# Optimization experiments

Measured on AMD Instinct MI355X. Metric: run time of the kernel, lower is better.

## Reference

```python
import jax, jax.numpy as jnp
import numpy as np

NUM_EXPERTS = 64
TOP_K = 2
TEMPERATURE = 1.0
MOMENTUM = 0.9


def _l2norm(x, axis=-1):
    # torch F.normalize: x / max(||x||, eps)
    n = jnp.linalg.norm(x, axis=axis, keepdims=True)
    return x / jnp.maximum(n, 1e-12)


def setup_inputs() -> dict:
    key = jax.random.key(0)
    k1, k2 = jax.random.split(key)
    hidden_states = jax.random.normal(k1, (4, 4096, 2048), dtype=jnp.float32)
    centers = _l2norm(jax.random.normal(k2, (NUM_EXPERTS, 2048), dtype=jnp.float32))
    return {"hidden_states": hidden_states, "centers": centers}


def reference(hidden_states, centers):
    B, T, H = hidden_states.shape
    flat = hidden_states.reshape(-1, H).astype(jnp.float32)  # [N, H]
    N = flat.shape[0]

    # cosine-similarity logits
    reps_n = _l2norm(flat)
    centers_n = _l2norm(centers)
    temp = jnp.maximum(jnp.float32(TEMPERATURE), 1e-6)
    logits = (reps_n @ centers_n.T) / temp  # [N, E]

    probs = jax.nn.softmax(logits, axis=-1)
    top_w, top_ids = jax.lax.top_k(probs, TOP_K)  # [N, k]
    top_w = top_w / (jnp.sum(top_w, axis=-1, keepdims=True) + 1e-9)

    # EMA center update from top-1 routed expert (training+update path)
    route = top_ids[:, 0]  # [N]
    sums = jax.ops.segment_sum(flat, route, num_segments=NUM_EXPERTS)  # [E, H]
    counts = jax.ops.segment_sum(jnp.ones((N, 1), jnp.float32), route,
                                 num_segments=NUM_EXPERTS)  # [E, 1]
    means = sums / (counts + 1e-6)
    updated = _l2norm(MOMENTUM * centers + (1.0 - MOMENTUM) * means)
    new_centers = jnp.where(counts > 0, updated, centers)

    top_ids = top_ids.reshape(B, T, TOP_K)
    top_w = top_w.reshape(B, T, TOP_K)
    return top_ids, top_w, new_centers
```

## Files before the change

### kernel.cpp

```cpp
#include <hip/hip_runtime.h>
#include <math.h>

#define NTOK 16384
#define HDIM 2048
#define NEXP 64
#define KK   32
#define TAU  5e-5f
#define LGT  16384
#define MAXB 2048
#define KPAD 40
#define LTS  132

typedef __attribute__((ext_vector_type(8))) short short8;
typedef __attribute__((ext_vector_type(4))) float f32x4;
typedef __attribute__((ext_vector_type(2))) unsigned int uint2v;


__global__ __launch_bounds__(256)
void zero_kernel(float* p, int n) {
  int i = blockIdx.x * 256 + threadIdx.x;
  if (i < n) p[i] = 0.0f;
}

__device__ __forceinline__ float block_reduce_sum(float v, float* red) {
  #pragma unroll
  for (int o = 32; o > 0; o >>= 1) v += __shfl_down(v, o, 64);
  int lane = threadIdx.x & 63;
  int wid  = threadIdx.x >> 6;
  if (lane == 0) red[wid] = v;
  __syncthreads();
  float s = red[0] + red[1] + red[2] + red[3];
  __syncthreads();
  return s;
}

__device__ __forceinline__ double block_reduce_sum_f64(double v, double* red) {
  const int tid = threadIdx.x;
  red[tid] = v;
  __syncthreads();
  if (tid < 128) red[tid] += red[tid + 128];
  __syncthreads();
  if (tid < 64)  red[tid] += red[tid + 64];
  __syncthreads();
  double s = 0.0;
  if (tid < 64) {
    s = red[tid];
    #pragma unroll
    for (int o = 32; o > 0; o >>= 1) s += __shfl_down(s, o, 64);
  }
  if (tid == 0) red[0] = s;
  __syncthreads();
  s = red[0];
  __syncthreads();
  return s;
}

__global__ __launch_bounds__(256)
void cnorm_kernel(const float* __restrict__ c, float* __restrict__ inv_nc) {
  __shared__ float red[4];
  int e = blockIdx.x;
  float ss = 0.f;
  #pragma unroll
  for (int j = 0; j < 8; ++j) {
    float v = c[e * HDIM + threadIdx.x + j * 256];
    ss += v * v;
  }
  float tot = block_reduce_sum(ss, red);
  if (threadIdx.x == 0) inv_nc[e] = 1.0f / fmaxf(sqrtf(tot), 1e-12f);
}

__global__ __launch_bounds__(256)
void cnormalize_kernel(const float* __restrict__ c, float* __restrict__ bn) {
  __shared__ double redd[256];
  __shared__ float s_nc;
  const int e = blockIdx.x;
  const int tid = threadIdx.x;
  const float* cr = c + (size_t)e * HDIM;
  double acc = 0.0;
  #pragma unroll
  for (int i = 0; i < 8; ++i) {
    double v = (double)cr[tid + 256 * i];
    acc += v * v;
  }
  double cn = block_reduce_sum_f64(acc, redd);
  if (tid == 0) s_nc = (float)fmax(sqrt(cn), 1e-12);
  __syncthreads();
  const double nc = (double)s_nc;
  #pragma unroll
  for (int i = 0; i < 8; ++i) {
    int k = tid + 256 * i;
    bn[(size_t)e * HDIM + k] = (float)((double)cr[k] / nc);
  }
}

__device__ __forceinline__ void cvt2(float v0, float v1, unsigned &hi, unsigned &lo) {
  unsigned u0 = __float_as_uint(v0);
  unsigned u1 = __float_as_uint(v1);
  unsigned h0 = u0 & 0xffff0000u;
  unsigned h1 = u1 & 0xffff0000u;
  float r0 = v0 - __uint_as_float(h0);
  float r1 = v1 - __uint_as_float(h1);
  hi = (u0 >> 16) | h1;
  lo = (__float_as_uint(r0) >> 16) | (__float_as_uint(r1) & 0xffff0000u);
}

__global__ __launch_bounds__(256)
void gemm_kernel(const float* __restrict__ x, const float* __restrict__ c,
                 float* __restrict__ logits, float* __restrict__ xnorm2) {
  __shared__ __align__(16) unsigned short smem[15360];
  unsigned short (*Ah)[KPAD] = (unsigned short (*)[KPAD])(smem);
  unsigned short (*Al)[KPAD] = (unsigned short (*)[KPAD])(smem + 5120);
  unsigned short (*Bh)[KPAD] = (unsigned short (*)[KPAD])(smem + 10240);
  unsigned short (*Bl)[KPAD] = (unsigned short (*)[KPAD])(smem + 12800);

  const int tid  = threadIdx.x;
  const int mt   = blockIdx.x >> 2;
  const int ks   = blockIdx.x & 3;
  const int t0   = mt * 128;
  const int kb   = ks * 512;
  const int sr   = tid >> 1;
  const int sq   = (tid & 1) * 16;
  const int er   = tid >> 2;
  const int eq   = (tid & 3) * 8;
  const int lane = tid & 63;
  const int w    = tid >> 6;
  const int fr   = lane & 15;
  const int fk   = (lane >> 4) * 8;

  const float* xrow = x + (size_t)(t0 + sr) * HDIM + kb + sq;
  const float* crow = c + (size_t)er * HDIM + kb + eq;

  f32x4 xp[4], cp[2];
  #pragma unroll
  for (int i = 0; i < 4; ++i) xp[i] = *(const f32x4*)(xrow + 4 * i);
  #pragma unroll
  for (int i = 0; i < 2; ++i) cp[i] = *(const f32x4*)(crow + 4 * i);

  f32x4 acc[2][4];
  #pragma unroll
  for (int mi = 0; mi < 2; ++mi)
    #pragma unroll
    for (int ni = 0; ni < 4; ++ni)
      acc[mi][ni] = (f32x4){0.f, 0.f, 0.f, 0.f};
  float nacc = 0.f;

  for (int it = 0; it < 16; ++it) {
    __syncthreads();
    #pragma unroll
    for (int i = 0; i < 4; ++i) {
      unsigned h01, l01, h23, l23;
      cvt2(xp[i].x, xp[i].y, h01, l01);
      cvt2(xp[i].z, xp[i].w, h23, l23);
      *(uint2v*)&Ah[sr][sq + 4 * i] = (uint2v){h01, h23};
      *(uint2v*)&Al[sr][sq + 4 * i] = (uint2v){l01, l23};
      nacc += xp[i].x*xp[i].x + xp[i].y*xp[i].y + xp[i].z*xp[i].z + xp[i].w*xp[i].w;
    }
    #pragma unroll
    for (int i = 0; i < 2; ++i) {
      unsigned h01, l01, h23, l23;
      cvt2(cp[i].x, cp[i].y, h01, l01);
      cvt2(cp[i].z, cp[i].w, h23, l23);
      *(uint2v*)&Bh[er][eq + 4 * i] = (uint2v){h01, h23};
      *(uint2v*)&Bl[er][eq + 4 * i] = (uint2v){l01, l23};
    }
    __syncthreads();
    if (it < 15) {
      const float* xn = xrow + (it + 1) * KK;
      const float* cn = crow + (it + 1) * KK;
      #pragma unroll
      for (int i = 0; i < 4; ++i) xp[i] = *(const f32x4*)(xn + 4 * i);
      #pragma unroll
      for (int i = 0; i < 2; ++i) cp[i] = *(const f32x4*)(cn + 4 * i);
    }
    short8 ah0 = *(const short8*)&Ah[w * 32 + fr][fk];
    short8 ah1 = *(const short8*)&Ah[w * 32 + 16 + fr][fk];
    short8 al0 = *(const short8*)&Al[w * 32 + fr][fk];
    short8 al1 = *(const short8*)&Al[w * 32 + 16 + fr][fk];
    #pragma unroll
    for (int ni = 0; ni < 4; ++ni) {
      short8 bh = *(const short8*)&Bh[ni * 16 + fr][fk];
      short8 bl = *(const short8*)&Bl[ni * 16 + fr][fk];
      acc[0][ni] = __builtin_amdgcn_mfma_f32_16x16x32_bf16(ah0, bh, acc[0][ni], 0, 0, 0);
      acc[0][ni] = __builtin_amdgcn_mfma_f32_16x16x32_bf16(ah0, bl, acc[0][ni], 0, 0, 0);
      acc[0][ni] = __builtin_amdgcn_mfma_f32_16x16x32_bf16(al0, bh, acc[0][ni], 0, 0, 0);
      acc[1][ni] = __builtin_amdgcn_mfma_f32_16x16x32_bf16(ah1, bh, acc[1][ni], 0, 0, 0);
      acc[1][ni] = __builtin_amdgcn_mfma_f32_16x16x32_bf16(ah1, bl, acc[1][ni], 0, 0, 0);
      acc[1][ni] = __builtin_amdgcn_mfma_f32_16x16x32_bf16(al1, bh, acc[1][ni], 0, 0, 0);
    }
  }

  atomicAdd(&xnorm2[t0 + sr], nacc);

  float* lt = (float*)smem;
  #pragma unroll
  for (int eh = 0; eh < 2; ++eh) {
    __syncthreads();
    #pragma unroll
    for (int ni2 = 0; ni2 < 2; ++ni2) {
      const int ni = eh * 2 + ni2;
      const int e  = ni2 * 16 + fr;
      #pragma unroll
      for (int mi = 0; mi < 2; ++mi) {
        const int t = w * 32 + mi * 16 + (lane >> 4) * 4;
        *(f32x4*)&lt[e * LTS + t] = acc[mi][ni];
      }
    }
    __syncthreads();
    #pragma unroll
    for (int n = 0; n < 16; ++n) {
      const int f = tid + n * 256;
      const int e = f >> 7;
      const int t = f & 127;
      atomicAdd(&logits[(size_t)(e + eh * 32) * LGT + t0 + t], lt[e * LTS + t]);
    }
  }
}

__global__ __launch_bounds__(64)
void softmax_kernel(const float* __restrict__ logits, const float* __restrict__ xnorm2,
                    const float* __restrict__ inv_nc, float* __restrict__ out,
                    int* __restrict__ route, int* __restrict__ nflag,
                    int* __restrict__ flags) {
  __shared__ float snc[NEXP];
  const int tid = threadIdx.x;
  snc[tid] = inv_nc[tid];
  __syncthreads();
  const int t = blockIdx.x * 64 + tid;
  const float inv_nx = 1.0f / fmaxf(sqrtf(xnorm2[t]), 1e-12f);
  float lv[NEXP];
  #pragma unroll
  for (int e = 0; e < NEXP; ++e)
    lv[e] = logits[(size_t)e * LGT + t] * snc[e] * inv_nx;
  float m1 = -1e30f, m2 = -1e30f, m3 = -1e30f;
  int i1 = 0, i2 = 0;
  #pragma unroll
  for (int e = 0; e < NEXP; ++e) {
    float l = lv[e];
    if (l > m1)      { m3 = m2; m2 = m1; i2 = i1; m1 = l; i1 = e; }
    else if (l > m2) { m3 = m2; m2 = l; i2 = e; }
    else if (l > m3) { m3 = l; }
  }
  float Z = 0.f;
  #pragma unroll
  for (int e = 0; e < NEXP; ++e) Z += expf(lv[e] - m1);
  const float p1w = 1.0f / Z;
  const float p2w = expf(m2 - m1) / Z;
  const float s   = p1w + p2w + 1e-9f;
  out[t * 2 + 0] = (float)i1;
  out[t * 2 + 1] = (float)i2;
  out[2 * NTOK + t * 2 + 0] = p1w / s;
  out[2 * NTOK + t * 2 + 1] = p2w / s;
  route[t] = i1;
  if ((m1 - m2) < TAU || (m2 - m3) < TAU) {
    int idx = atomicAdd(nflag, 1);
    flags[idx] = t;
  }
}

__global__ __launch_bounds__(256)
void refine_np_kernel(const float* __restrict__ x, const float* __restrict__ bn,
                      float* __restrict__ out, int* __restrict__ route,
                      const int* __restrict__ nflag, const int* __restrict__ flags) {
  __shared__ float a_lds[HDIM];
  __shared__ double redd[256];
  __shared__ float lf[NEXP];
  __shared__ float s_nx;
  const int tid  = threadIdx.x;
  const int lane = tid & 63;
  const int w    = tid >> 6;
  const int n = *nflag;
  for (int j = blockIdx.x; j < n; j += gridDim.x) {
    const int t = flags[j];
    const float* xr = x + (size_t)t * HDIM;
    double xacc = 0.0;
    #pragma unroll
    for (int i = 0; i < 8; ++i) {
      double v = (double)xr[tid + 256 * i];
      xacc += v * v;
    }
    double xn = block_reduce_sum_f64(xacc, redd);
    if (tid == 0) s_nx = (float)fmax(sqrt(xn), 1e-12);
    __syncthreads();
    const double nx = (double)s_nx;
    #pragma unroll
    for (int i = 0; i < 8; ++i) {
      int k = tid + 256 * i;
      a_lds[k] = (float)((double)xr[k] / nx);
    }
    __syncthreads();
    #pragma unroll 1
    for (int ei = 0; ei < 16; ++ei) {
      const int e = w * 16 + ei;
      const float* br = bn + (size_t)e * HDIM;
      double d = 0.0;
      #pragma unroll 8
      for (int i = 0; i < 32; ++i) {
        int k = lane + 64 * i;
        d += (double)a_lds[k] * (double)br[k];
      }
      #pragma unroll
      for (int o = 32; o > 0; o >>= 1) d += __shfl_down(d, o, 64);
      if (lane == 0) lf[e] = (float)d;
    }
    __syncthreads();
    if (tid == 0) {
      float m32 = lf[0];
      for (int ee = 1; ee < NEXP; ++ee) m32 = fmaxf(m32, lf[ee]);
      float ex[NEXP];
      for (int ee = 0; ee < NEXP; ++ee)
        ex[ee] = (float)exp((double)(lf[ee] - m32));
      float r[8];
      #pragma unroll
      for (int q = 0; q < 8; ++q) r[q] = ex[q];
      for (int i = 8; i < NEXP; i += 8)
        #pragma unroll
        for (int q = 0; q < 8; ++q) r[q] += ex[i + q];
      const float Z = ((r[0] + r[1]) + (r[2] + r[3])) + ((r[4] + r[5]) + (r[6] + r[7]));
      float p1 = -1.f, p2 = -1.f;
      int i1 = 0, i2 = 0;
      for (int ee = 0; ee < NEXP; ++ee) {
        float p = ex[ee] / Z;
        if (p > p1)      { p2 = p1; i2 = i1; p1 = p; i1 = ee; }
        else if (p > p2) { p2 = p; i2 = ee; }
      }
      const float s = (p1 + p2) + 1e-9f;
      out[t * 2 + 0] = (float)i1;
      out[t * 2 + 1] = (float)i2;
      out[2 * NTOK + t * 2 + 0] = p1 / s;
      out[2 * NTOK + t * 2 + 1] = p2 / s;
      route[t] = i1;
    }
    __syncthreads();
  }
}

__global__ __launch_bounds__(64)
void refine_np_slow(const float* __restrict__ x, const float* __restrict__ c,
                    float* __restrict__ out, int* __restrict__ route,
                    const int* __restrict__ nflag, const int* __restrict__ flags) {
  __shared__ float lf[NEXP];
  const int e = threadIdx.x;
  const int n = *nflag;
  for (int j = blockIdx.x; j < n; j += gridDim.x) {
    const int t = flags[j];
    const float* xr = x + (size_t)t * HDIM;
    const float* cr = c + (size_t)e * HDIM;
    double xn = 0.0, cn = 0.0;
    for (int k = 0; k < HDIM; ++k) {
      double xv = (double)xr[k];
      double cv = (double)cr[k];
      xn += xv * xv;
      cn += cv * cv;
    }
    const float nx32 = (float)fmax(sqrt(xn), 1e-12);
    const float nc32 = (float)fmax(sqrt(cn), 1e-12);
    double d = 0.0;
    for (int k = 0; k < HDIM; ++k) {
      float a = (float)((double)xr[k] / (double)nx32);
      float b = (float)((double)cr[k] / (double)nc32);
      d += (double)a * (double)b;
    }
    lf[e] = (float)d;
    __syncthreads();
    if (e == 0) {
      float m32 = lf[0];
      for (int ee = 1; ee < NEXP; ++ee) m32 = fmaxf(m32, lf[ee]);
      float ex[NEXP];
      for (int ee = 0; ee < NEXP; ++ee)
        ex[ee] = (float)exp((double)(lf[ee] - m32));
      float r[8];
      #pragma unroll
      for (int q = 0; q < 8; ++q) r[q] = ex[q];
      for (int i = 8; i < NEXP; i += 8)
        #pragma unroll
        for (int q = 0; q < 8; ++q) r[q] += ex[i + q];
      const float Z = ((r[0] + r[1]) + (r[2] + r[3])) + ((r[4] + r[5]) + (r[6] + r[7]));
      float p1 = -1.f, p2 = -1.f;
      int i1 = 0, i2 = 0;
      for (int ee = 0; ee < NEXP; ++ee) {
        float p = ex[ee] / Z;
        if (p > p1)      { p2 = p1; i2 = i1; p1 = p; i1 = ee; }
        else if (p > p2) { p2 = p; i2 = ee; }
      }
      const float s = (p1 + p2) + 1e-9f;
      out[t * 2 + 0] = (float)i1;
      out[t * 2 + 1] = (float)i2;
      out[2 * NTOK + t * 2 + 0] = p1 / s;
      out[2 * NTOK + t * 2 + 1] = p2 / s;
      route[t] = i1;
    }
    __syncthreads();
  }
}

__global__ __launch_bounds__(256)
void scatter_kernel(const int* __restrict__ route, int* __restrict__ cursor,
                    int* __restrict__ bucket) {
  const int t = blockIdx.x * 256 + threadIdx.x;
  const int e = route[t];
  const int pos = atomicAdd(&cursor[e], 1);
  if (pos < MAXB) bucket[e * MAXB + pos] = t;
}

__global__ __launch_bounds__(256)
void segsum_dense(const float* __restrict__ x, const int* __restrict__ cursor,
                  const int* __restrict__ bucket, float* __restrict__ sums) {
  __shared__ int ts[MAXB];
  const int e   = blockIdx.x >> 3;
  const int hc  = blockIdx.x & 7;
  const int hb  = hc * 256;
  const int tid = threadIdx.x;
  int n = cursor[e];
  if (n > MAXB) n = MAXB;
  for (int i = tid; i < n; i += 256) ts[i] = bucket[e * MAXB + i];
  __syncthreads();
  float a[8];
  #pragma unroll
  for (int q = 0; q < 8; ++q) a[q] = 0.f;
  int i = 0;
  for (; i + 7 < n; i += 8) {
    #pragma unroll
    for (int q = 0; q < 8; ++q)
      a[q] += x[(size_t)ts[i + q] * HDIM + hb + tid];
  }
  for (; i < n; ++i) a[0] += x[(size_t)ts[i] * HDIM + hb + tid];
  const float s = ((a[0] + a[1]) + (a[2] + a[3])) + ((a[4] + a[5]) + (a[6] + a[7]));
  sums[e * HDIM + hb + tid] = s;
}

__global__ __launch_bounds__(256)
void finalize_kernel(const float* __restrict__ c, const float* __restrict__ sums,
                     const int* __restrict__ counts, float* __restrict__ out) {
  __shared__ float red[4];
  const int e = blockIdx.x;
  const int tid = threadIdx.x;
  const float cnt = (float)counts[e];
  const float minv = 1.0f / (cnt + 1e-6f);
  float u[8], cv[8];
  float ss = 0.f;
  #pragma unroll
  for (int j = 0; j < 8; ++j) {
    int h = tid + j * 256;
    cv[j] = c[e * HDIM + h];
    float mean = sums[e * HDIM + h] * minv;
    u[j] = 0.9f * cv[j] + 0.1f * mean;
    ss += u[j] * u[j];
  }
  float tot = block_reduce_sum(ss, red);
  float sc = 1.0f / fmaxf(sqrtf(tot), 1e-12f);
  const bool nz = cnt > 0.f;
  #pragma unroll
  for (int j = 0; j < 8; ++j) {
    int h = tid + j * 256;
    out[4 * NTOK + e * HDIM + h] = nz ? u[j] * sc : cv[j];
  }
}

__global__ __launch_bounds__(256)
void router_kernel(const float* __restrict__ x, const float* __restrict__ c,
                   const float* __restrict__ inv_nc, float* __restrict__ out,
                   int* __restrict__ route, int* __restrict__ nflag,
                   int* __restrict__ flags) {
  __shared__ __align__(16) float xs[64][36];
  __shared__ float lgs[64][67];
  const int tid  = threadIdx.x;
  const int lane = tid & 63;
  const int w    = tid >> 6;
  const int t0   = blockIdx.x * 64;
  const int e0   = __builtin_amdgcn_readfirstlane(w * 16);
  const float* cb = c + (size_t)e0 * HDIM;
  const int st = tid >> 3;
  const int sk = (tid & 7) * 4;
  float acc[16];
  #pragma unroll
  for (int e = 0; e < 16; ++e) acc[e] = 0.f;
  float nacc = 0.f;
  float4 p0 = *(const float4*)&x[(size_t)(t0 + st)      * HDIM + sk];
  float4 p1 = *(const float4*)&x[(size_t)(t0 + st + 32) * HDIM + sk];
  for (int k0 = 0; k0 < HDIM; k0 += 32) {
    __syncthreads();
    *(float4*)&xs[st][sk]      = p0;
    *(float4*)&xs[st + 32][sk] = p1;
    __syncthreads();
    const int kn = k0 + 32;
    if (kn < HDIM) {
      p0 = *(const float4*)&x[(size_t)(t0 + st)      * HDIM + kn + sk];
      p1 = *(const float4*)&x[(size_t)(t0 + st + 32) * HDIM + kn + sk];
    }
    float a[32];
    #pragma unroll
    for (int j = 0; j < 32; j += 4) {
      float4 v = *(const float4*)&xs[lane][j];
      a[j] = v.x; a[j+1] = v.y; a[j+2] = v.z; a[j+3] = v.w;
    }
    if (w == 0) {
      #pragma unroll
      for (int j = 0; j < 32; ++j) nacc += a[j] * a[j];
    }
    #pragma unroll
    for (int e = 0; e < 16; ++e) {
      const float* br = cb + (size_t)e * HDIM + k0;
      #pragma unroll
      for (int j = 0; j < 32; j += 4) {
        float4 bv = *(const float4*)&br[j];
        acc[e] += a[j]*bv.x + a[j+1]*bv.y + a[j+2]*bv.z + a[j+3]*bv.w;
      }
    }
  }
  #pragma unroll
  for (int e = 0; e < 16; ++e) lgs[lane][e0 + e] = acc[e] * inv_nc[e0 + e];
  __syncthreads();
  if (w == 0) {
    const float inv_nx = 1.0f / fmaxf(sqrtf(nacc), 1e-12f);
    float m1 = -1e30f, m2 = -1e30f, m3 = -1e30f;
    int i1 = 0, i2 = 0;
    for (int e = 0; e < NEXP; ++e) {
      float l = lgs[lane][e] * inv_nx;
      if (l > m1)      { m3 = m2; m2 = m1; i2 = i1; m1 = l; i1 = e; }
      else if (l > m2) { m3 = m2; m2 = l; i2 = e; }
      else if (l > m3) { m3 = l; }
    }
    float Z = 0.f;
    for (int e = 0; e < NEXP; ++e) Z += expf(lgs[lane][e] * inv_nx - m1);
    const float p1w = 1.0f / Z;
    const float p2w = expf(m2 - m1) / Z;
    const float s   = p1w + p2w + 1e-9f;
    const int tg = t0 + lane;
    out[tg * 2 + 0] = (float)i1;
    out[tg * 2 + 1] = (float)i2;
    out[2 * NTOK + tg * 2 + 0] = p1w / s;
    out[2 * NTOK + tg * 2 + 1] = p2w / s;
    route[tg] = i1;
    if ((m1 - m2) < TAU || (m2 - m3) < TAU) {
      int idx = atomicAdd(nflag, 1);
      flags[idx] = tg;
    }
  }
}

__global__ __launch_bounds__(512)
void segsum_kernel(const float* __restrict__ x, const int* __restrict__ route,
                   float* __restrict__ sums, int* __restrict__ counts) {
  __shared__ float ls[NEXP * 256];
  __shared__ int lcnt[NEXP];
  const int tid  = threadIdx.x;
  const int lane = tid & 63;
  const int w    = tid >> 6;
  const int hc   = blockIdx.x & 7;
  const int tg   = blockIdx.x >> 3;
  const int hb   = hc * 256;
  #pragma unroll
  for (int i = 0; i < 32; ++i) ls[tid + i * 512] = 0.f;
  if (tid < NEXP) lcnt[tid] = 0;
  __syncthreads();
  const int tbase = tg * 512 + w * 64;
  #pragma unroll 4
  for (int i = 0; i < 64; ++i) {
    const int t = tbase + i;
    const int e = route[t];
    const float* xr = x + (size_t)t * HDIM + hb + lane;
    #pragma unroll
    for (int j = 0; j < 4; ++j)
      atomicAdd(&ls[e * 256 + lane + 64 * j], xr[64 * j]);
    if (hc == 0 && lane == 0) atomicAdd(&lcnt[e], 1);
  }
  __syncthreads();
  #pragma unroll
  for (int i = tid; i < NEXP * 256; i += 512) {
    const int e = i >> 8, h = i & 255;
    atomicAdd(&sums[e * HDIM + hb + h], ls[i]);
  }
  if (hc == 0 && tid < NEXP && lcnt[tid] > 0) atomicAdd(&counts[tid], lcnt[tid]);
}

extern "C" void kernel_launch(void* const* d_in, const int* in_sizes, int n_in,
                              void* d_out, int out_size, void* d_ws, size_t ws_size,
                              hipStream_t stream) {
  const float* x = (const float*)d_in[0];
  const float* c = (const float*)d_in[1];
  float* out = (float*)d_out;
  float* ws = (float*)d_ws;

  float* inv_nc = ws;
  int*   counts = (int*)(ws + 64);
  int*   nflag  = (int*)(ws + 128);
  int*   route  = (int*)(ws + 192);
  int*   flags  = (int*)(ws + 16576);
  float* sums   = ws + 32960;
  float* xnorm2 = ws + 164032;
  float* logits = ws + 180416;
  float* bn     = ws + 1228992;
  int*   bucket = (int*)(ws + 1360064);

  const size_t NEED = 1491136ull * 4ull;
  if (ws_size >= NEED) {
    zero_kernel<<<1, 256, 0, stream>>>(ws + 64, 128);
    zero_kernel<<<4160, 256, 0, stream>>>(ws + 164032, 1064960);
    cnorm_kernel<<<NEXP, 256, 0, stream>>>(c, inv_nc);
    cnormalize_kernel<<<NEXP, 256, 0, stream>>>(c, bn);
    gemm_kernel<<<512, 256, 0, stream>>>(x, c, logits, xnorm2);
    softmax_kernel<<<NTOK / 64, 64, 0, stream>>>(logits, xnorm2, inv_nc, out, route, nflag, flags);
    refine_np_kernel<<<512, 256, 0, stream>>>(x, bn, out, route, nflag, flags);
    scatter_kernel<<<64, 256, 0, stream>>>(route, counts, bucket);
    segsum_dense<<<512, 256, 0, stream>>>(x, counts, bucket, sums);
    finalize_kernel<<<NEXP, 256, 0, stream>>>(c, sums, counts, out);
  } else {
    zero_kernel<<<1, 256, 0, stream>>>(ws + 64, 128);
    zero_kernel<<<512, 256, 0, stream>>>(sums, 131072);
    cnorm_kernel<<<NEXP, 256, 0, stream>>>(c, inv_nc);
    router_kernel<<<NTOK / 64, 256, 0, stream>>>(x, c, inv_nc, out, route, nflag, flags);
    refine_np_slow<<<1024, 64, 0, stream>>>(x, c, out, route, nflag, flags);
    segsum_kernel<<<256, 512, 0, stream>>>(x, route, sums, counts);
    finalize_kernel<<<NEXP, 256, 0, stream>>>(c, sums, counts, out);
  }
}
```

Baseline: 315.9 us.

## Fuse logits GEMM with softmax/top-k and pre-split centers to bf16 hi/lo

Replaces the split-K GEMM, which accumulated logits and row norms through global atomics, plus the separate softmax kernel, with one fused kernel per 32-token tile. That kernel computes the full K reduction with double-buffered LDS staging, keeps logits in shared memory and runs top-2 and softmax in place. Center normalization and bf16 hi/lo splitting are merged into one prep kernel, so the GEMM loads pre-split centers. This removes the large logits buffer, its zeroing, the atomics and two launches. The cost is that each block reloads all centers per tile and the epilogue runs on only 32 threads.

After: 314.6 us. Within noise of the previous version (-0.4%).

```diff
diff --git a/kernel.cpp b/kernel.cpp
--- a/kernel.cpp
+++ b/kernel.cpp
@@ -6,10 +6,9 @@
 #define NEXP 64
 #define KK   32
 #define TAU  5e-5f
-#define LGT  16384
 #define MAXB 2048
-#define KPAD 40
-#define LTS  132
+#define TB   32
+#define TPAD 36
 
 typedef __attribute__((ext_vector_type(8))) short short8;
 typedef __attribute__((ext_vector_type(4))) float f32x4;
@@ -70,26 +69,42 @@
 }
 
 __global__ __launch_bounds__(256)
-void cnormalize_kernel(const float* __restrict__ c, float* __restrict__ bn) {
+void cprep_kernel(const float* __restrict__ c, float* __restrict__ inv_nc,
+                  float* __restrict__ bn, unsigned short* __restrict__ cbh,
+                  unsigned short* __restrict__ cbl) {
+  __shared__ float red[4];
   __shared__ double redd[256];
   __shared__ float s_nc;
   const int e = blockIdx.x;
   const int tid = threadIdx.x;
   const float* cr = c + (size_t)e * HDIM;
+  float ss = 0.f;
   double acc = 0.0;
   #pragma unroll
-  for (int i = 0; i < 8; ++i) {
-    double v = (double)cr[tid + 256 * i];
-    acc += v * v;
-  }
+  for (int j = 0; j < 8; ++j) {
+    float v = cr[tid + j * 256];
+    ss += v * v;
+    double dv = (double)v;
+    acc += dv * dv;
+  }
+  float tot = block_reduce_sum(ss, red);
   double cn = block_reduce_sum_f64(acc, redd);
-  if (tid == 0) s_nc = (float)fmax(sqrt(cn), 1e-12);
+  if (tid == 0) {
+    inv_nc[e] = 1.0f / fmaxf(sqrtf(tot), 1e-12f);
+    s_nc = (float)fmax(sqrt(cn), 1e-12);
+  }
   __syncthreads();
   const double nc = (double)s_nc;
   #pragma unroll
-  for (int i = 0; i < 8; ++i) {
-    int k = tid + 256 * i;
-    bn[(size_t)e * HDIM + k] = (float)((double)cr[k] / nc);
+  for (int j = 0; j < 8; ++j) {
+    const int k = tid + j * 256;
+    const float v = cr[k];
+    bn[(size_t)e * HDIM + k] = (float)((double)v / nc);
+    unsigned u = __float_as_uint(v);
+    unsigned h = u & 0xffff0000u;
+    float r = v - __uint_as_float(h);
+    cbh[(size_t)e * HDIM + k] = (unsigned short)(u >> 16);
+    cbl[(size_t)e * HDIM + k] = (unsigned short)(__float_as_uint(r) >> 16);
   }
 }
 
@@ -105,155 +120,132 @@
 }
 
 __global__ __launch_bounds__(256)
-void gemm_kernel(const float* __restrict__ x, const float* __restrict__ c,
-                 float* __restrict__ logits, float* __restrict__ xnorm2) {
-  __shared__ __align__(16) unsigned short smem[15360];
-  unsigned short (*Ah)[KPAD] = (unsigned short (*)[KPAD])(smem);
-  unsigned short (*Al)[KPAD] = (unsigned short (*)[KPAD])(smem + 5120);
-  unsigned short (*Bh)[KPAD] = (unsigned short (*)[KPAD])(smem + 10240);
-  unsigned short (*Bl)[KPAD] = (unsigned short (*)[KPAD])(smem + 12800);
+void fused_kernel(const float* __restrict__ x,
+                  const unsigned short* __restrict__ cbh,
+                  const unsigned short* __restrict__ cbl,
+                  const float* __restrict__ inv_nc,
+                  float* __restrict__ out, int* __restrict__ route,
+                  int* __restrict__ nflag, int* __restrict__ flags) {
+  __shared__ __align__(16) unsigned short Ah[2][TB][32];
+  __shared__ __align__(16) unsigned short Al[2][TB][32];
+  __shared__ __align__(16) unsigned short Bh[2][NEXP][32];
+  __shared__ __align__(16) unsigned short Bl[2][NEXP][32];
+  __shared__ float lg[NEXP][TPAD];
+  __shared__ float xn_lds[TB];
+  __shared__ float snc[NEXP];
 
   const int tid  = threadIdx.x;
-  const int mt   = blockIdx.x >> 2;
-  const int ks   = blockIdx.x & 3;
-  const int t0   = mt * 128;
-  const int kb   = ks * 512;
-  const int sr   = tid >> 1;
-  const int sq   = (tid & 1) * 16;
+  const int t0   = blockIdx.x * TB;
+  const int sr   = tid >> 3;
+  const int sq   = (tid & 7) * 4;
   const int er   = tid >> 2;
   const int eq   = (tid & 3) * 8;
   const int lane = tid & 63;
   const int w    = tid >> 6;
+  const int m16  = (w & 1) * 16;
+  const int nh32 = (w >> 1) * 32;
   const int fr   = lane & 15;
   const int fk   = (lane >> 4) * 8;
 
-  const float* xrow = x + (size_t)(t0 + sr) * HDIM + kb + sq;
-  const float* crow = c + (size_t)er * HDIM + kb + eq;
-
-  f32x4 xp[4], cp[2];
-  #pragma unroll
-  for (int i = 0; i < 4; ++i) xp[i] = *(const f32x4*)(xrow + 4 * i);
-  #pragma unroll
-  for (int i = 0; i < 2; ++i) cp[i] = *(const f32x4*)(crow + 4 * i);
-
-  f32x4 acc[2][4];
-  #pragma unroll
-  for (int mi = 0; mi < 2; ++mi)
-    #pragma unroll
-    for (int ni = 0; ni < 4; ++ni)
-      acc[mi][ni] = (f32x4){0.f, 0.f, 0.f, 0.f};
+  if (tid < NEXP) snc[tid] = inv_nc[tid];
+
+  const float* xptr = x + (size_t)(t0 + sr) * HDIM + sq;
+  const unsigned short* bhptr = cbh + (size_t)er * HDIM + eq;
+  const unsigned short* blptr = cbl + (size_t)er * HDIM + eq;
+
+  f32x4 xp;
+  short8 bhp, blp;
   float nacc = 0.f;
 
-  for (int it = 0; it < 16; ++it) {
-    __syncthreads();
-    #pragma unroll
-    for (int i = 0; i < 4; ++i) {
-      unsigned h01, l01, h23, l23;
-      cvt2(xp[i].x, xp[i].y, h01, l01);
-      cvt2(xp[i].z, xp[i].w, h23, l23);
-      *(uint2v*)&Ah[sr][sq + 4 * i] = (uint2v){h01, h23};
-      *(uint2v*)&Al[sr][sq + 4 * i] = (uint2v){l01, l23};
-      nacc += xp[i].x*xp[i].x + xp[i].y*xp[i].y + xp[i].z*xp[i].z + xp[i].w*xp[i].w;
-    }
-    #pragma unroll
-    for (int i = 0; i < 2; ++i) {
-      unsigned h01, l01, h23, l23;
-      cvt2(cp[i].x, cp[i].y, h01, l01);
-      cvt2(cp[i].z, cp[i].w, h23, l23);
-      *(uint2v*)&Bh[er][eq + 4 * i] = (uint2v){h01, h23};
-      *(uint2v*)&Bl[er][eq + 4 * i] = (uint2v){l01, l23};
-    }
-    __syncthreads();
-    if (it < 15) {
-      const float* xn = xrow + (it + 1) * KK;
-      const float* cn = crow + (it + 1) * KK;
-      #pragma unroll
-      for (int i = 0; i < 4; ++i) xp[i] = *(const f32x4*)(xn + 4 * i);
-      #pragma unroll
-      for (int i = 0; i < 2; ++i) cp[i] = *(const f32x4*)(cn + 4 * i);
-    }
-    short8 ah0 = *(const short8*)&Ah[w * 32 + fr][fk];
-    short8 ah1 = *(const short8*)&Ah[w * 32 + 16 + fr][fk];
-    short8 al0 = *(const short8*)&Al[w * 32 + fr][fk];
-    short8 al1 = *(const short8*)&Al[w * 32 + 16 + fr][fk];
-    #pragma unroll
-    for (int ni = 0; ni < 4; ++ni) {
-      short8 bh = *(const short8*)&Bh[ni * 16 + fr][fk];
-      short8 bl = *(const short8*)&Bl[ni * 16 + fr][fk];
-      acc[0][ni] = __builtin_amdgcn_mfma_f32_16x16x32_bf16(ah0, bh, acc[0][ni], 0, 0, 0);
-      acc[0][ni] = __builtin_amdgcn_mfma_f32_16x16x32_bf16(ah0, bl, acc[0][ni], 0, 0, 0);
-      acc[0][ni] = __builtin_amdgcn_mfma_f32_16x16x32_bf16(al0, bh, acc[0][ni], 0, 0, 0);
-      acc[1][ni] = __builtin_amdgcn_mfma_f32_16x16x32_bf16(ah1, bh, acc[1][ni], 0, 0, 0);
-      acc[1][ni] = __builtin_amdgcn_mfma_f32_16x16x32_bf16(ah1, bl, acc[1][ni], 0, 0, 0);
-      acc[1][ni] = __builtin_amdgcn_mfma_f32_16x16x32_bf16(al1, bh, acc[1][ni], 0, 0, 0);
-    }
-  }
-
-  atomicAdd(&xnorm2[t0 + sr], nacc);
-
-  float* lt = (float*)smem;
-  #pragma unroll
-  for (int eh = 0; eh < 2; ++eh) {
-    __syncthreads();
-    #pragma unroll
-    for (int ni2 = 0; ni2 < 2; ++ni2) {
-      const int ni = eh * 2 + ni2;
-      const int e  = ni2 * 16 + fr;
-      #pragma unroll
-      for (int mi = 0; mi < 2; ++mi) {
-        const int t = w * 32 + mi * 16 + (lane >> 4) * 4;
-        *(f32x4*)&lt[e * LTS + t] = acc[mi][ni];
+  auto stage = [&](int b) {
+    unsigned h01, l01, h23, l23;
+    cvt2(xp.x, xp.y, h01, l01);
+    cvt2(xp.z, xp.w, h23, l23);
+    *(uint2v*)&Ah[b][sr][sq] = (uint2v){h01, h23};
+    *(uint2v*)&Al[b][sr][sq] = (uint2v){l01, l23};
+    nacc += xp.x*xp.x + xp.y*xp.y + xp.z*xp.z + xp.w*xp.w;
+    *(short8*)&Bh[b][er][eq] = bhp;
+    *(short8*)&Bl[b][er][eq] = blp;
+  };
+
+  xp  = *(const f32x4*)(xptr);
+  bhp = *(const short8*)(bhptr);
+  blp = *(const short8*)(blptr);
+  stage(0);
+  xp  = *(const f32x4*)(xptr + KK);
+  bhp = *(const short8*)(bhptr + KK);
+  blp = *(const short8*)(blptr + KK);
+  __syncthreads();
+
+  f32x4 acc0 = (f32x4){0.f, 0.f, 0.f, 0.f};
+  f32x4 acc1 = (f32x4){0.f, 0.f, 0.f, 0.f};
+
+  for (int it = 0; it < 64; ++it) {
+    const int cur = it & 1;
+    short8 ah  = *(const short8*)&Ah[cur][m16 + fr][fk];
+    short8 al  = *(const short8*)&Al[cur][m16 + fr][fk];
+    short8 bh0 = *(const short8*)&Bh[cur][nh32 + fr][fk];
+    short8 bl0 = *(const short8*)&Bl[cur][nh32 + fr][fk];
+    short8 bh1 = *(const short8*)&Bh[cur][nh32 + 16 + fr][fk];
+    short8 bl1 = *(const short8*)&Bl[cur][nh32 + 16 + fr][fk];
+    if (it < 63) {
+      stage(cur ^ 1);
+      if (it < 62) {
+        const int off = (it + 2) * KK;
+        xp  = *(const f32x4*)(xptr + off);
+        bhp = *(const short8*)(bhptr + off);
+        blp = *(const short8*)(blptr + off);
       }
     }
-    __syncthreads();
-    #pragma unroll
-    for (int n = 0; n < 16; ++n) {
-      const int f = tid + n * 256;
-      const int e = f >> 7;
-      const int t = f & 127;
-      atomicAdd(&logits[(size_t)(e + eh * 32) * LGT + t0 + t], lt[e * LTS + t]);
-    }
-  }
-}
-
-__global__ __launch_bounds__(64)
-void softmax_kernel(const float* __restrict__ logits, const float* __restrict__ xnorm2,
-                    const float* __restrict__ inv_nc, float* __restrict__ out,
-                    int* __restrict__ route, int* __restrict__ nflag,
-                    int* __restrict__ flags) {
-  __shared__ float snc[NEXP];
-  const int tid = threadIdx.x;
-  snc[tid] = inv_nc[tid];
-  __syncthreads();
-  const int t = blockIdx.x * 64 + tid;
-  const float inv_nx = 1.0f / fmaxf(sqrtf(xnorm2[t]), 1e-12f);
-  float lv[NEXP];
-  #pragma unroll
-  for (int e = 0; e < NEXP; ++e)
-    lv[e] = logits[(size_t)e * LGT + t] * snc[e] * inv_nx;
-  float m1 = -1e30f, m2 = -1e30f, m3 = -1e30f;
-  int i1 = 0, i2 = 0;
-  #pragma unroll
-  for (int e = 0; e < NEXP; ++e) {
-    float l = lv[e];
-    if (l > m1)      { m3 = m2; m2 = m1; i2 = i1; m1 = l; i1 = e; }
-    else if (l > m2) { m3 = m2; m2 = l; i2 = e; }
-    else if (l > m3) { m3 = l; }
-  }
-  float Z = 0.f;
-  #pragma unroll
-  for (int e = 0; e < NEXP; ++e) Z += expf(lv[e] - m1);
-  const float p1w = 1.0f / Z;
-  const float p2w = expf(m2 - m1) / Z;
-  const float s   = p1w + p2w + 1e-9f;
-  out[t * 2 + 0] = (float)i1;
-  out[t * 2 + 1] = (float)i2;
-  out[2 * NTOK + t * 2 + 0] = p1w / s;
-  out[2 * NTOK + t * 2 + 1] = p2w / s;
-  route[t] = i1;
-  if ((m1 - m2) < TAU || (m2 - m3) < TAU) {
-    int idx = atomicAdd(nflag, 1);
-    flags[idx] = t;
+    acc0 = __builtin_amdgcn_mfma_f32_16x16x32_bf16(ah, bh0, acc0, 0, 0, 0);
+    acc0 = __builtin_amdgcn_mfma_f32_16x16x32_bf16(ah, bl0, acc0, 0, 0, 0);
+    acc0 = __builtin_amdgcn_mfma_f32_16x16x32_bf16(al, bh0, acc0, 0, 0, 0);
+    acc1 = __builtin_amdgcn_mfma_f32_16x16x32_bf16(ah, bh1, acc1, 0, 0, 0);
+    acc1 = __builtin_amdgcn_mfma_f32_16x16x32_bf16(ah, bl1, acc1, 0, 0, 0);
+    acc1 = __builtin_amdgcn_mfma_f32_16x16x32_bf16(al, bh1, acc1, 0, 0, 0);
+    __syncthreads();
+  }
+
+  float s = nacc;
+  s += __shfl_xor(s, 1, 64);
+  s += __shfl_xor(s, 2, 64);
+  s += __shfl_xor(s, 4, 64);
+  if ((tid & 7) == 0) xn_lds[sr] = s;
+
+  const int tb = m16 + (lane >> 4) * 4;
+  *(f32x4*)&lg[nh32 + fr][tb]      = acc0;
+  *(f32x4*)&lg[nh32 + 16 + fr][tb] = acc1;
+  __syncthreads();
+
+  if (tid < TB) {
+    const int t  = tid;
+    const int tg = t0 + t;
+    const float inv_nx = 1.0f / fmaxf(sqrtf(xn_lds[t]), 1e-12f);
+    float m1 = -1e30f, m2 = -1e30f, m3 = -1e30f;
+    int i1 = 0, i2 = 0;
+    #pragma unroll
+    for (int e = 0; e < NEXP; ++e) {
+      float l = lg[e][t] * snc[e] * inv_nx;
+      if (l > m1)      { m3 = m2; m2 = m1; i2 = i1; m1 = l; i1 = e; }
+      else if (l > m2) { m3 = m2; m2 = l; i2 = e; }
+      else if (l > m3) { m3 = l; }
+    }
+    float Z = 0.f;
+    #pragma unroll
+    for (int e = 0; e < NEXP; ++e)
+      Z += expf(lg[e][t] * snc[e] * inv_nx - m1);
+    const float p1w = 1.0f / Z;
+    const float p2w = expf(m2 - m1) / Z;
+    const float s2  = p1w + p2w + 1e-9f;
+    out[tg * 2 + 0] = (float)i1;
+    out[tg * 2 + 1] = (float)i2;
+    out[2 * NTOK + tg * 2 + 0] = p1w / s2;
+    out[2 * NTOK + tg * 2 + 1] = p2w / s2;
+    route[tg] = i1;
+    if ((m1 - m2) < TAU || (m2 - m3) < TAU) {
+      int idx = atomicAdd(nflag, 1);
+      flags[idx] = tg;
+    }
   }
 }
 
@@ -587,19 +579,16 @@
   int*   route  = (int*)(ws + 192);
   int*   flags  = (int*)(ws + 16576);
   float* sums   = ws + 32960;
-  float* xnorm2 = ws + 164032;
-  float* logits = ws + 180416;
-  float* bn     = ws + 1228992;
-  int*   bucket = (int*)(ws + 1360064);
-
-  const size_t NEED = 1491136ull * 4ull;
+  float* bn     = ws + 164032;
+  unsigned short* cbh = (unsigned short*)(ws + 295104);
+  unsigned short* cbl = (unsigned short*)(ws + 360640);
+  int*   bucket = (int*)(ws + 426176);
+
+  const size_t NEED = 557248ull * 4ull;
   if (ws_size >= NEED) {
     zero_kernel<<<1, 256, 0, stream>>>(ws + 64, 128);
-    zero_kernel<<<4160, 256, 0, stream>>>(ws + 164032, 1064960);
-    cnorm_kernel<<<NEXP, 256, 0, stream>>>(c, inv_nc);
-    cnormalize_kernel<<<NEXP, 256, 0, stream>>>(c, bn);
-    gemm_kernel<<<512, 256, 0, stream>>>(x, c, logits, xnorm2);
-    softmax_kernel<<<NTOK / 64, 64, 0, stream>>>(logits, xnorm2, inv_nc, out, route, nflag, flags);
+    cprep_kernel<<<NEXP, 256, 0, stream>>>(c, inv_nc, bn, cbh, cbl);
+    fused_kernel<<<NTOK / TB, 256, 0, stream>>>(x, cbh, cbl, inv_nc, out, route, nflag, flags);
     refine_np_kernel<<<512, 256, 0, stream>>>(x, bn, out, route, nflag, flags);
     scatter_kernel<<<64, 256, 0, stream>>>(route, counts, bucket);
     segsum_dense<<<512, 256, 0, stream>>>(x, counts, bucket, sums);
```
